# Optimization experiments

Hardware: AMD Instinct MI355X
Metric: run time of the kernel (lower is better)

## Reference

```python
import jax, jax.numpy as jnp
import numpy as np

N = 50000      # nodes
E = 800000     # edges (avg degree 16)
IN = 128       # input feature dim
D = 128        # state_size
B = 10         # bounding_parameter
L = 4          # num_layers
OUT = 40       # out_channels
A = 10.0       # config.a (sigmoid sharpness)


def setup_inputs() -> dict:
    key = jax.random.key(0)
    ks = jax.random.split(key, 6)
    x = jax.random.normal(ks[0], (N, IN), dtype=jnp.float32)
    edge_index = jax.random.randint(ks[1], (2, E), 0, N, dtype=jnp.int64)
    W_in = jax.random.normal(ks[2], (IN, D), dtype=jnp.float32) * 0.05
    b_in = jnp.zeros((D,), jnp.float32)
    W_layers = jax.random.normal(ks[3], (L, D * (B + 1), D), dtype=jnp.float32) * 0.05
    b_layers = jnp.zeros((L, D), jnp.float32)
    W_out = jax.random.normal(ks[4], ((L + 1) * D, OUT), dtype=jnp.float32) * 0.05
    b_out = jnp.zeros((OUT,), jnp.float32)
    return dict(x=x, edge_index=edge_index, W_in=W_in, b_in=b_in,
                W_layers=W_layers, b_layers=b_layers, W_out=W_out, b_out=b_out)


def diff_argmax(x):
    # straight-through argmax: value is one-hot, grad flows through softmax
    y_soft = jax.nn.softmax(x, axis=-1)
    y_hard = jax.nn.one_hot(jnp.argmax(y_soft, axis=-1), x.shape[-1], dtype=x.dtype)
    return jax.lax.stop_gradient(y_hard - y_soft) + y_soft


def reference(x, edge_index, W_in, b_in, W_layers, b_layers, W_out, b_out):
    src, dst = edge_index[0], edge_index[1]
    y_range = jnp.arange(B, dtype=jnp.float32)

    # input layer (LINEAR) + differentiable argmax
    h = diff_argmax(x @ W_in + b_in)          # [N, D]
    xs = [h]
    for l in range(L):
        # scatter-add message aggregation: sum_j x_j over incoming edges
        msg = jax.ops.segment_sum(h[src], dst, num_segments=N)   # [N, D]
        clamped = jnp.clip(msg, 0.0, float(B))
        # bounded expansion: soft thresholds at 0..B-1
        states = jax.nn.sigmoid(A * (jax.nn.elu(clamped[..., None] - y_range) - 0.5))
        states = states.reshape(N, D * B)
        combined = jnp.concatenate([h, states], axis=1)          # [N, D*(B+1)]
        h = diff_argmax(combined @ W_layers[l] + b_layers[l])    # [N, D]
        xs.append(h)

    hcat = jnp.concatenate(xs, axis=1)                           # [N, (L+1)*D]
    logits = jax.nn.log_softmax(hcat @ W_out + b_out, axis=-1)   # [N, OUT]
    return logits
```

## Files before the change

kernel.cpp:

```cpp
#include <hip/hip_runtime.h>
#include <math.h>

#define NN 50000
#define NE 800000
#define DD 128
#define LL 4
#define OUTD 40
#define NPART 8
#define PART_SZ ((NN + NPART - 1) / NPART)
#define NCHUNK 256
#define CHUNK_E (NE / NCHUNK)
#define NB_IN ((NN + 63) / 64)
#define NB_T 256
#define NB_SC (NPART * NCHUNK)
#define MAXD 96

__device__ __forceinline__ float S_func(float t) {
    float z = (t > 0.0f) ? t : expm1f(t);
    float xx = 10.0f * (z - 0.5f);
    return 1.0f / (1.0f + expf(-xx));
}

__global__ __launch_bounds__(256) void front_kernel(
        const float* __restrict__ W_layers, float* __restrict__ T0,
        float* __restrict__ Delta,
        const float* __restrict__ x, const float* __restrict__ W_in,
        const float* __restrict__ b_in, int* __restrict__ idx0,
        const int* __restrict__ src, const int* __restrict__ dst,
        unsigned int* __restrict__ cursor, int* __restrict__ slots) {
    __shared__ float wlds[16][128];
    __shared__ float xls[64][20];
    int t = threadIdx.x;

    if (blockIdx.x >= NB_IN) {
        if (blockIdx.x < NB_IN + NB_T) {
            int bd = (blockIdx.x - NB_IN) * 2 + (t >> 7);
            int l = bd >> 7, d = bd & 127;
            int j = t & 127;
            const float* W2 = W_layers + ((size_t)l * 1408 + 128 + (size_t)d * 10) * 128;
            float w[10];
            #pragma unroll
            for (int y = 0; y < 10; ++y) w[y] = W2[(size_t)y * 128 + j];
            float t0 = 0.0f;
            #pragma unroll
            for (int y = 0; y < 10; ++y) t0 += S_func((float)(0 - y)) * w[y];
            T0[(size_t)bd * 128 + j] = t0;
            for (int c = 1; c <= 10; ++c) {
                float tc = 0.0f;
                #pragma unroll
                for (int y = 0; y < 10; ++y) tc += S_func((float)(c - y)) * w[y];
                Delta[((size_t)bd * 10 + (c - 1)) * 128 + j] = tc - t0;
            }
        } else {
            int bb = blockIdx.x - NB_IN - NB_T;
            int part = bb & (NPART - 1);
            int chunk = bb >> 3;
            int lo = part * PART_SZ, hi = lo + PART_SZ;
            int e0 = chunk * CHUNK_E, e1 = e0 + CHUNK_E;
            for (int e = e0 + t; e < e1; e += 256) {
                int d = dst[e];
                int s = src[e];
                if (d >= lo && d < hi) {
                    unsigned int pos = atomicAdd(&cursor[d], 1u);
                    if (pos < MAXD) slots[(size_t)d * MAXD + pos] = s;
                }
            }
        }
        return;
    }

    int bb = blockIdx.x;
    int cg = t & 15;
    int ng = t >> 4;
    int n0 = bb * 64;
    float acc[4][8];
    #pragma unroll
    for (int i = 0; i < 4; ++i)
        #pragma unroll
        for (int r = 0; r < 8; ++r) acc[i][r] = 0.0f;

    for (int kc = 0; kc < 8; ++kc) {
        __syncthreads();
        #pragma unroll
        for (int p = 0; p < 2; ++p) {
            int f = t + p * 256;
            int kr = f >> 5, c4 = f & 31;
            *(float4*)&wlds[kr][c4 * 4] =
                *(const float4*)&W_in[(size_t)(kc * 16 + kr) * 128 + c4 * 4];
        }
        {
            int node = t >> 2, k4 = t & 3;
            int gn = n0 + node;
            if (gn > NN - 1) gn = NN - 1;
            *(float4*)&xls[node][k4 * 4] =
                *(const float4*)&x[(size_t)gn * 128 + kc * 16 + k4 * 4];
        }
        __syncthreads();
        #pragma unroll
        for (int kk4 = 0; kk4 < 4; ++kk4) {
            float4 xv[4];
            #pragma unroll
            for (int i = 0; i < 4; ++i)
                xv[i] = *(const float4*)&xls[ng * 4 + i][kk4 * 4];
            #pragma unroll
            for (int q = 0; q < 4; ++q) {
                int k = kk4 * 4 + q;
                float4 w1 = *(const float4*)&wlds[k][cg * 4];
                float4 w2 = *(const float4*)&wlds[k][64 + cg * 4];
                #pragma unroll
                for (int i = 0; i < 4; ++i) {
                    float xvv = (q == 0) ? xv[i].x : (q == 1) ? xv[i].y
                              : (q == 2) ? xv[i].z : xv[i].w;
                    acc[i][0] = fmaf(xvv, w1.x, acc[i][0]);
                    acc[i][1] = fmaf(xvv, w1.y, acc[i][1]);
                    acc[i][2] = fmaf(xvv, w1.z, acc[i][2]);
                    acc[i][3] = fmaf(xvv, w1.w, acc[i][3]);
                    acc[i][4] = fmaf(xvv, w2.x, acc[i][4]);
                    acc[i][5] = fmaf(xvv, w2.y, acc[i][5]);
                    acc[i][6] = fmaf(xvv, w2.z, acc[i][6]);
                    acc[i][7] = fmaf(xvv, w2.w, acc[i][7]);
                }
            }
        }
    }
    float4 b1 = *(const float4*)&b_in[cg * 4];
    float4 b2 = *(const float4*)&b_in[64 + cg * 4];
    #pragma unroll
    for (int i = 0; i < 4; ++i) {
        float v0 = acc[i][0] + b1.x, v1 = acc[i][1] + b1.y;
        float v2 = acc[i][2] + b1.z, v3 = acc[i][3] + b1.w;
        float v4 = acc[i][4] + b2.x, v5 = acc[i][5] + b2.y;
        float v6 = acc[i][6] + b2.z, v7 = acc[i][7] + b2.w;
        float bv = v0; int bi = cg * 4;
        if (v1 > bv) { bv = v1; bi = cg * 4 + 1; }
        if (v2 > bv) { bv = v2; bi = cg * 4 + 2; }
        if (v3 > bv) { bv = v3; bi = cg * 4 + 3; }
        if (v4 > bv) { bv = v4; bi = 64 + cg * 4; }
        if (v5 > bv) { bv = v5; bi = 64 + cg * 4 + 1; }
        if (v6 > bv) { bv = v6; bi = 64 + cg * 4 + 2; }
        if (v7 > bv) { bv = v7; bi = 64 + cg * 4 + 3; }
        #pragma unroll
        for (int o = 8; o >= 1; o >>= 1) {
            float ov = __shfl_xor(bv, o);
            int oi = __shfl_xor(bi, o);
            if (ov > bv || (ov == bv && oi < bi)) { bv = ov; bi = oi; }
        }
        int n = n0 + ng * 4 + i;
        if (cg == 0 && n < NN) idx0[n] = bi;
    }
}

__global__ void build_Base(const float* __restrict__ T0, float* __restrict__ Base) {
    int l = blockIdx.x, j = threadIdx.x;
    float s = 0.0f;
    for (int d = 0; d < 128; ++d) s += T0[((size_t)l * 128 + d) * 128 + j];
    Base[l * 128 + j] = s;
}

__global__ __launch_bounds__(256) void layer_kernel(
        const unsigned int* __restrict__ cursor, const int* __restrict__ slots,
        const float* __restrict__ Wl, const float* __restrict__ bl,
        const float* __restrict__ Delta_l, const float* __restrict__ Base_l,
        const int* __restrict__ idx_in, int* __restrict__ idx_out) {
    __shared__ unsigned int cnt[8][128];
    __shared__ int list[8][128];
    int w = threadIdx.x >> 6;
    int lane = threadIdx.x & 63;
    int h = lane >> 5, l = lane & 31;
    int nidx = w * 2 + h;
    int n = blockIdx.x * 8 + nidx;
    unsigned int deg = cursor[n];
    if (deg > MAXD) deg = MAXD;
    int hidx = idx_in[n];
    float4 wv = *(const float4*)((const char*)Wl + (size_t)hidx * 512 + l * 16);
    float4 bs = *(const float4*)((const char*)Base_l + l * 16);
    float4 bb = *(const float4*)((const char*)bl + l * 16);
    cnt[nidx][l]      = 0u;
    cnt[nidx][l + 32] = 0u;
    cnt[nidx][l + 64] = 0u;
    cnt[nidx][l + 96] = 0u;
    const int* srow = slots + (size_t)n * MAXD;
    for (unsigned int e = l; e < deg; e += 32u) {
        int s = srow[e];
        atomicAdd(&cnt[nidx][idx_in[s]], 1u);
    }
    unsigned int c0 = cnt[nidx][4 * l];
    unsigned int c1 = cnt[nidx][4 * l + 1];
    unsigned int c2 = cnt[nidx][4 * l + 2];
    unsigned int c3 = cnt[nidx][4 * l + 3];
    int f0 = c0 != 0u, f1 = c1 != 0u, f2 = c2 != 0u, f3 = c3 != 0u;
    int nb = f0 + f1 + f2 + f3;
    int incl = nb;
    #pragma unroll
    for (int o = 1; o < 32; o <<= 1) {
        int u = __shfl_up(incl, o, 32);
        if (l >= o) incl += u;
    }
    int pos = incl - nb;
    int total = __shfl(incl, 31, 32);
    if (f0) { unsigned int cc = c0 > 10u ? 10u : c0;
              list[nidx][pos++] = (int)(((4 * l + 0) * 10 + (int)cc - 1) * 512); }
    if (f1) { unsigned int cc = c1 > 10u ? 10u : c1;
              list[nidx][pos++] = (int)(((4 * l + 1) * 10 + (int)cc - 1) * 512); }
    if (f2) { unsigned int cc = c2 > 10u ? 10u : c2;
              list[nidx][pos++] = (int)(((4 * l + 2) * 10 + (int)cc - 1) * 512); }
    if (f3) { unsigned int cc = c3 > 10u ? 10u : c3;
              list[nidx][pos++] = (int)(((4 * l + 3) * 10 + (int)cc - 1) * 512); }
    float4 acc;
    acc.x = wv.x + bs.x;
    acc.y = wv.y + bs.y;
    acc.z = wv.z + bs.z;
    acc.w = wv.w + bs.w;
    const char* Db = (const char*)Delta_l + l * 16;
    int i = 0;
    for (; i + 8 <= total; i += 8) {
        int o0 = list[nidx][i];
        int o1 = list[nidx][i + 1];
        int o2 = list[nidx][i + 2];
        int o3 = list[nidx][i + 3];
        int o4 = list[nidx][i + 4];
        int o5 = list[nidx][i + 5];
        int o6 = list[nidx][i + 6];
        int o7 = list[nidx][i + 7];
        float4 d0 = *(const float4*)(Db + o0);
        float4 d1 = *(const float4*)(Db + o1);
        float4 d2 = *(const float4*)(Db + o2);
        float4 d3 = *(const float4*)(Db + o3);
        float4 d4 = *(const float4*)(Db + o4);
        float4 d5 = *(const float4*)(Db + o5);
        float4 d6 = *(const float4*)(Db + o6);
        float4 d7 = *(const float4*)(Db + o7);
        acc.x += d0.x; acc.y += d0.y; acc.z += d0.z; acc.w += d0.w;
        acc.x += d1.x; acc.y += d1.y; acc.z += d1.z; acc.w += d1.w;
        acc.x += d2.x; acc.y += d2.y; acc.z += d2.z; acc.w += d2.w;
        acc.x += d3.x; acc.y += d3.y; acc.z += d3.z; acc.w += d3.w;
        acc.x += d4.x; acc.y += d4.y; acc.z += d4.z; acc.w += d4.w;
        acc.x += d5.x; acc.y += d5.y; acc.z += d5.z; acc.w += d5.w;
        acc.x += d6.x; acc.y += d6.y; acc.z += d6.z; acc.w += d6.w;
        acc.x += d7.x; acc.y += d7.y; acc.z += d7.z; acc.w += d7.w;
    }
    for (; i + 4 <= total; i += 4) {
        int o0 = list[nidx][i];
        int o1 = list[nidx][i + 1];
        int o2 = list[nidx][i + 2];
        int o3 = list[nidx][i + 3];
        float4 d0 = *(const float4*)(Db + o0);
        float4 d1 = *(const float4*)(Db + o1);
        float4 d2 = *(const float4*)(Db + o2);
        float4 d3 = *(const float4*)(Db + o3);
        acc.x += d0.x; acc.y += d0.y; acc.z += d0.z; acc.w += d0.w;
        acc.x += d1.x; acc.y += d1.y; acc.z += d1.z; acc.w += d1.w;
        acc.x += d2.x; acc.y += d2.y; acc.z += d2.z; acc.w += d2.w;
        acc.x += d3.x; acc.y += d3.y; acc.z += d3.z; acc.w += d3.w;
    }
    for (; i < total; ++i) {
        float4 dv = *(const float4*)(Db + list[nidx][i]);
        acc.x += dv.x; acc.y += dv.y; acc.z += dv.z; acc.w += dv.w;
    }
    acc.x += bb.x; acc.y += bb.y; acc.z += bb.z; acc.w += bb.w;
    float bv = acc.x; int bi = 4 * l;
    if (acc.y > bv) { bv = acc.y; bi = 4 * l + 1; }
    if (acc.z > bv) { bv = acc.z; bi = 4 * l + 2; }
    if (acc.w > bv) { bv = acc.w; bi = 4 * l + 3; }
    #pragma unroll
    for (int o = 16; o >= 1; o >>= 1) {
        float ov = __shfl_xor(bv, o);
        int oi = __shfl_xor(bi, o);
        if (ov > bv || (ov == bv && oi < bi)) { bv = ov; bi = oi; }
    }
    if (l == 0) idx_out[n] = bi;
}

__global__ __launch_bounds__(256) void output_kernel(const int* __restrict__ idx,
        const float* __restrict__ W_out, const float* __restrict__ b_out,
        float* __restrict__ out) {
    int w = threadIdx.x >> 6;
    int o = threadIdx.x & 63;
    int n = blockIdx.x * 4 + w;
    if (n >= NN) return;
    float v;
    if (o < OUTD) {
        float a = 0.0f;
        #pragma unroll
        for (int l = 0; l < 5; ++l) {
            int id = idx[(size_t)l * NN + n];
            a += W_out[((size_t)(l * 128 + id)) * OUTD + o];
        }
        v = a + b_out[o];
    } else {
        v = -INFINITY;
    }
    float mx = v;
    #pragma unroll
    for (int s = 32; s >= 1; s >>= 1) mx = fmaxf(mx, __shfl_xor(mx, s));
    float e = (o < OUTD) ? expf(v - mx) : 0.0f;
    float se = e;
    #pragma unroll
    for (int s = 32; s >= 1; s >>= 1) se += __shfl_xor(se, s);
    if (o < OUTD) out[(size_t)n * OUTD + o] = v - mx - logf(se);
}

extern "C" void kernel_launch(void* const* d_in, const int* in_sizes, int n_in,
                              void* d_out, int out_size, void* d_ws, size_t ws_size,
                              hipStream_t stream) {
    const float* x        = (const float*)d_in[0];
    const int*   edge     = (const int*)d_in[1];
    const float* W_in     = (const float*)d_in[2];
    const float* b_in     = (const float*)d_in[3];
    const float* W_layers = (const float*)d_in[4];
    const float* b_layers = (const float*)d_in[5];
    const float* W_out    = (const float*)d_in[6];
    const float* b_out    = (const float*)d_in[7];
    float* out = (float*)d_out;

    char* ws = (char*)d_ws;
    size_t off = 0;
    float* Delta = (float*)(ws + off); off += (size_t)LL * 128 * 10 * 128 * 4;
    float* T0    = (float*)(ws + off); off += (size_t)LL * 128 * 128 * 4;
    float* Base  = (float*)(ws + off); off += (size_t)LL * 128 * 4;
    int*   idx   = (int*)(ws + off);   off += (size_t)(LL + 1) * NN * 4;
    unsigned int* cursor = (unsigned int*)(ws + off); off += (size_t)NN * 4;
    int*   slots = (int*)(ws + off);   off += (size_t)NN * MAXD * 4;

    const int* srcp = edge;
    const int* dstp = edge + NE;

    hipMemsetAsync(cursor, 0, (size_t)NN * 4, stream);
    hipLaunchKernelGGL(front_kernel, dim3(NB_IN + NB_T + NB_SC), dim3(256), 0, stream,
                       W_layers, T0, Delta, x, W_in, b_in, idx, srcp, dstp, cursor, slots);
    hipLaunchKernelGGL(build_Base, dim3(LL), dim3(128), 0, stream, T0, Base);

    for (int l = 0; l < LL; ++l) {
        hipLaunchKernelGGL(layer_kernel, dim3(NN / 8), dim3(256), 0, stream,
                           cursor, slots,
                           W_layers + (size_t)l * 1408 * 128,
                           b_layers + (size_t)l * 128,
                           Delta + (size_t)l * 128 * 10 * 128,
                           Base + (size_t)l * 128,
                           idx + (size_t)l * NN,
                           idx + (size_t)(l + 1) * NN);
    }
    hipLaunchKernelGGL(output_kernel, dim3((NN + 3) / 4), dim3(256), 0, stream,
                       idx, W_out, b_out, out);
}
```

Baseline: 204.1 us.

## Stage count-one Delta rows in LDS with larger 1024-thread layer blocks

The layer kernel now runs 1024-thread blocks covering 32 nodes each. Every block copies the 128 count-one Delta rows (64 KB) into shared memory. List entries with count one carry a tag bit and are read from LDS, while other counts still read Delta from global memory. This targets the scattered global gathers for the most common count value. In exchange, each block reloads 64 KB per launch, needs about 96 KB of LDS, which limits occupancy, and the 8-wide unrolled gather loop becomes a 4-wide loop with a branch per entry.

```diff
diff --git a/kernel.cpp b/kernel.cpp
--- a/kernel.cpp
+++ b/kernel.cpp
@@ -157,28 +157,38 @@
     Base[l * 128 + j] = s;
 }
 
-__global__ __launch_bounds__(256) void layer_kernel(
+__global__ __launch_bounds__(1024) void layer_kernel(
         const unsigned int* __restrict__ cursor, const int* __restrict__ slots,
         const float* __restrict__ Wl, const float* __restrict__ bl,
         const float* __restrict__ Delta_l, const float* __restrict__ Base_l,
         const int* __restrict__ idx_in, int* __restrict__ idx_out) {
-    __shared__ unsigned int cnt[8][128];
-    __shared__ int list[8][128];
-    int w = threadIdx.x >> 6;
-    int lane = threadIdx.x & 63;
-    int h = lane >> 5, l = lane & 31;
-    int nidx = w * 2 + h;
-    int n = blockIdx.x * 8 + nidx;
+    __shared__ float D1[128][128];
+    __shared__ unsigned int cnt[32][128];
+    __shared__ int list[32][128];
+    int t = threadIdx.x;
+    #pragma unroll
+    for (int p = 0; p < 4; ++p) {
+        int f = t + p * 1024;
+        int row = f >> 5, c4 = f & 31;
+        *(float4*)&D1[row][c4 * 4] =
+            *(const float4*)&Delta_l[(size_t)row * 10 * 128 + c4 * 4];
+    }
+    int nidx = t >> 5;
+    int l = t & 31;
+    int n = blockIdx.x * 32 + nidx;
+    cnt[nidx][l]      = 0u;
+    cnt[nidx][l + 32] = 0u;
+    cnt[nidx][l + 64] = 0u;
+    cnt[nidx][l + 96] = 0u;
+    __syncthreads();
+    if (n >= NN) return;
+
     unsigned int deg = cursor[n];
     if (deg > MAXD) deg = MAXD;
     int hidx = idx_in[n];
     float4 wv = *(const float4*)((const char*)Wl + (size_t)hidx * 512 + l * 16);
     float4 bs = *(const float4*)((const char*)Base_l + l * 16);
     float4 bb = *(const float4*)((const char*)bl + l * 16);
-    cnt[nidx][l]      = 0u;
-    cnt[nidx][l + 32] = 0u;
-    cnt[nidx][l + 64] = 0u;
-    cnt[nidx][l + 96] = 0u;
     const int* srow = slots + (size_t)n * MAXD;
     for (unsigned int e = l; e < deg; e += 32u) {
         int s = srow[e];
@@ -198,63 +208,43 @@
     }
     int pos = incl - nb;
     int total = __shfl(incl, 31, 32);
-    if (f0) { unsigned int cc = c0 > 10u ? 10u : c0;
-              list[nidx][pos++] = (int)(((4 * l + 0) * 10 + (int)cc - 1) * 512); }
-    if (f1) { unsigned int cc = c1 > 10u ? 10u : c1;
-              list[nidx][pos++] = (int)(((4 * l + 1) * 10 + (int)cc - 1) * 512); }
-    if (f2) { unsigned int cc = c2 > 10u ? 10u : c2;
-              list[nidx][pos++] = (int)(((4 * l + 2) * 10 + (int)cc - 1) * 512); }
-    if (f3) { unsigned int cc = c3 > 10u ? 10u : c3;
-              list[nidx][pos++] = (int)(((4 * l + 3) * 10 + (int)cc - 1) * 512); }
+    if (f0) { unsigned int cc = c0 > 10u ? 10u : c0; int d = 4 * l;
+              list[nidx][pos++] = (cc == 1u) ? ((d << 9) | 1)
+                                             : ((d * 10 + (int)cc - 1) << 9); }
+    if (f1) { unsigned int cc = c1 > 10u ? 10u : c1; int d = 4 * l + 1;
+              list[nidx][pos++] = (cc == 1u) ? ((d << 9) | 1)
+                                             : ((d * 10 + (int)cc - 1) << 9); }
+    if (f2) { unsigned int cc = c2 > 10u ? 10u : c2; int d = 4 * l + 2;
+              list[nidx][pos++] = (cc == 1u) ? ((d << 9) | 1)
+                                             : ((d * 10 + (int)cc - 1) << 9); }
+    if (f3) { unsigned int cc = c3 > 10u ? 10u : c3; int d = 4 * l + 3;
+              list[nidx][pos++] = (cc == 1u) ? ((d << 9) | 1)
+                                             : ((d * 10 + (int)cc - 1) << 9); }
     float4 acc;
     acc.x = wv.x + bs.x;
     acc.y = wv.y + bs.y;
     acc.z = wv.z + bs.z;
     acc.w = wv.w + bs.w;
-    const char* Db = (const char*)Delta_l + l * 16;
+    const char* Dg = (const char*)Delta_l + l * 16;
+    const char* Dl = (const char*)D1 + l * 16;
     int i = 0;
-    for (; i + 8 <= total; i += 8) {
-        int o0 = list[nidx][i];
-        int o1 = list[nidx][i + 1];
-        int o2 = list[nidx][i + 2];
-        int o3 = list[nidx][i + 3];
-        int o4 = list[nidx][i + 4];
-        int o5 = list[nidx][i + 5];
-        int o6 = list[nidx][i + 6];
-        int o7 = list[nidx][i + 7];
-        float4 d0 = *(const float4*)(Db + o0);
-        float4 d1 = *(const float4*)(Db + o1);
-        float4 d2 = *(const float4*)(Db + o2);
-        float4 d3 = *(const float4*)(Db + o3);
-        float4 d4 = *(const float4*)(Db + o4);
-        float4 d5 = *(const float4*)(Db + o5);
-        float4 d6 = *(const float4*)(Db + o6);
-        float4 d7 = *(const float4*)(Db + o7);
+    for (; i + 4 <= total; i += 4) {
+        int e0 = list[nidx][i];
+        int e1 = list[nidx][i + 1];
+        int e2 = list[nidx][i + 2];
+        int e3 = list[nidx][i + 3];
+        float4 d0 = (e0 & 1) ? *(const float4*)(Dl + (e0 & ~1)) : *(const float4*)(Dg + e0);
+        float4 d1 = (e1 & 1) ? *(const float4*)(Dl + (e1 & ~1)) : *(const float4*)(Dg + e1);
+        float4 d2 = (e2 & 1) ? *(const float4*)(Dl + (e2 & ~1)) : *(const float4*)(Dg + e2);
+        float4 d3 = (e3 & 1) ? *(const float4*)(Dl + (e3 & ~1)) : *(const float4*)(Dg + e3);
         acc.x += d0.x; acc.y += d0.y; acc.z += d0.z; acc.w += d0.w;
         acc.x += d1.x; acc.y += d1.y; acc.z += d1.z; acc.w += d1.w;
         acc.x += d2.x; acc.y += d2.y; acc.z += d2.z; acc.w += d2.w;
         acc.x += d3.x; acc.y += d3.y; acc.z += d3.z; acc.w += d3.w;
-        acc.x += d4.x; acc.y += d4.y; acc.z += d4.z; acc.w += d4.w;
-        acc.x += d5.x; acc.y += d5.y; acc.z += d5.z; acc.w += d5.w;
-        acc.x += d6.x; acc.y += d6.y; acc.z += d6.z; acc.w += d6.w;
-        acc.x += d7.x; acc.y += d7.y; acc.z += d7.z; acc.w += d7.w;
-    }
-    for (; i + 4 <= total; i += 4) {
-        int o0 = list[nidx][i];
-        int o1 = list[nidx][i + 1];
-        int o2 = list[nidx][i + 2];
-        int o3 = list[nidx][i + 3];
-        float4 d0 = *(const float4*)(Db + o0);
-        float4 d1 = *(const float4*)(Db + o1);
-        float4 d2 = *(const float4*)(Db + o2);
-        float4 d3 = *(const float4*)(Db + o3);
-        acc.x += d0.x; acc.y += d0.y; acc.z += d0.z; acc.w += d0.w;
-        acc.x += d1.x; acc.y += d1.y; acc.z += d1.z; acc.w += d1.w;
-        acc.x += d2.x; acc.y += d2.y; acc.z += d2.z; acc.w += d2.w;
-        acc.x += d3.x; acc.y += d3.y; acc.z += d3.z; acc.w += d3.w;
     }
     for (; i < total; ++i) {
-        float4 dv = *(const float4*)(Db + list[nidx][i]);
+        int e = list[nidx][i];
+        float4 dv = (e & 1) ? *(const float4*)(Dl + (e & ~1)) : *(const float4*)(Dg + e);
         acc.x += dv.x; acc.y += dv.y; acc.z += dv.z; acc.w += dv.w;
     }
     acc.x += bb.x; acc.y += bb.y; acc.z += bb.z; acc.w += bb.w;
@@ -331,7 +321,7 @@
     hipLaunchKernelGGL(build_Base, dim3(LL), dim3(128), 0, stream, T0, Base);
 
     for (int l = 0; l < LL; ++l) {
-        hipLaunchKernelGGL(layer_kernel, dim3(NN / 8), dim3(256), 0, stream,
+        hipLaunchKernelGGL(layer_kernel, dim3((NN + 31) / 32), dim3(1024), 0, stream,
                            cursor, slots,
                            W_layers + (size_t)l * 1408 * 128,
                            b_layers + (size_t)l * 128,
```

After: 244.5 us. 1.2x slower.
